# Kernel optimization log

Hardware: AMD Instinct MI355X
Metric: run time of the kernel (lower is better)

The kernel has to match this reference:

```python
import jax, jax.numpy as jnp
import numpy as np

B, L, H = 32, 512, 1024
H2 = H // 2          # split half = 512
D_ATTN = 64
EPS = 1e-5


def setup_inputs() -> dict:
    key = jax.random.key(0)
    ks = jax.random.split(key, 6)
    x = jax.random.normal(ks[0], (B, L, H), dtype=jnp.float32)
    # LayerNorm params (default torch init: weight=1, bias=0)
    ln_gamma = jnp.ones((H2,), jnp.float32)
    ln_beta = jnp.zeros((H2,), jnp.float32)
    # Toeplitz params (module inits w_vector=0, bias=1; use small random w for nontrivial math)
    w_vector = jax.random.normal(ks[1], (2 * L - 1,), jnp.float32) * 0.02
    t_bias = jnp.ones((L,), jnp.float32)
    # TinyAttention: kqv Linear(H2 -> 3*d_attn), proj Linear(d_attn -> H2)
    kqv_w = jax.random.normal(ks[2], (H2, 3 * D_ATTN), jnp.float32) * 0.02
    kqv_b = jnp.zeros((3 * D_ATTN,), jnp.float32)
    proj_w = jax.random.normal(ks[3], (D_ATTN, H2), jnp.float32) * 0.02
    proj_b = jnp.zeros((H2,), jnp.float32)
    return {"x": x, "ln_gamma": ln_gamma, "ln_beta": ln_beta,
            "w_vector": w_vector, "t_bias": t_bias,
            "kqv_w": kqv_w, "kqv_b": kqv_b, "proj_w": proj_w, "proj_b": proj_b}


def _toeplitz(w_vector):
    # Faithful replication of get_toeplitz(): pad, tile, trim, reshape, crop.
    r = w_vector.shape[0] // 2            # = L - 1
    t = jnp.pad(w_vector, (0, L))         # length 3L - 1
    t = jnp.tile(t, L)[:-L]               # length L * (3L - 2)
    t = t.reshape(L, 3 * L - 2)
    return t[:, r:-r]                      # [L, L]


def _tiny_attention(v, kqv_w, kqv_b, proj_w, proj_b):
    kqv = v @ kqv_w + kqv_b                        # [B, L, 3*d_attn]
    k, q, val = jnp.split(kqv, 3, axis=-1)         # chunk order: key, query, value
    scale = 1.0 / jnp.sqrt(jnp.float32(q.shape[-1]))
    scores = jnp.einsum('bqd,bkd->bqk', q, k) * scale
    soft = jax.nn.softmax(scores, axis=-1)
    head = jnp.einsum('bqk,bkd->bqd', soft, val)   # [B, L, d_attn]
    return head @ proj_w + proj_b                  # [B, L, H2]


def reference(x, ln_gamma, ln_beta, w_vector, t_bias, kqv_w, kqv_b, proj_w, proj_b):
    u, v = jnp.split(x, 2, axis=-1)                # each [B, L, H2]
    head = _tiny_attention(v, kqv_w, kqv_b, proj_w, proj_b)
    # LayerNorm over last dim
    mu = jnp.mean(v, axis=-1, keepdims=True)
    var = jnp.mean(jnp.square(v - mu), axis=-1, keepdims=True)
    vn = (v - mu) * jax.lax.rsqrt(var + EPS) * ln_gamma + ln_beta
    # spatial (Toeplitz) mixing: permute -> [B, H2, L], matmul [L, L], bias
    w_t = _toeplitz(w_vector)
    vm = jnp.einsum('blc,lm->bmc', vn, w_t.T).transpose(0, 2, 1)  # keep faithful: vp @ w_t
    vm = jnp.einsum('bcl,lm->bcm', vn.transpose(0, 2, 1), w_t) + t_bias
    v_out = vm.transpose(0, 2, 1) + head           # [B, L, H2]
    return u * v_out
```

## Files before the change

kernel.cpp:

```cpp
#include <hip/hip_runtime.h>
#include <math.h>

#define NB 32
#define LL 512
#define HH 1024
#define H2 512
#define DA 64

typedef unsigned int u32;
typedef unsigned short u16;
typedef __bf16 bf16x8 __attribute__((ext_vector_type(8)));
typedef float f32x4 __attribute__((ext_vector_type(4)));
typedef u16 u16x8 __attribute__((ext_vector_type(8)));

__device__ __forceinline__ u16 f2bu(float f) {
    u32 u = __builtin_bit_cast(u32, f);
    u = (u + 0x7fff + ((u >> 16) & 1)) >> 16;
    return (u16)u;
}

__device__ __forceinline__ float b2f(u16 u) {
    u32 v = (u32)u << 16;
    return __builtin_bit_cast(float, v);
}

__device__ __forceinline__ void async_cp16(const void* g, void* l) {
    __builtin_amdgcn_global_load_lds(
        (const __attribute__((address_space(1))) u32*)g,
        (__attribute__((address_space(3))) u32*)l, 16, 0, 0);
}

__global__ void prep_kernel(const float* __restrict__ wv,
                            const float* __restrict__ kqvw,
                            const float* __restrict__ projw,
                            u16* __restrict__ wt, u16* __restrict__ kqvwT,
                            u16* __restrict__ projwT) {
    int e = blockIdx.x * 256 + threadIdx.x;
    if (e < 262144) {
        int m = e >> 9, l = e & 511;
        wt[e] = f2bu(wv[511 + m - l]);
    } else if (e < 262144 + 98304) {
        int i = e - 262144;
        int n = i >> 9, k = i & 511;
        kqvwT[i] = f2bu(kqvw[(size_t)k * 192 + n]);
    } else {
        int i = e - 360448;
        int c = i >> 6, d = i & 63;
        projwT[i] = f2bu(projw[(size_t)d * 512 + c]);
    }
}

__global__ __launch_bounds__(256, 2)
void v_kernel(const float* __restrict__ x,
              const u16* __restrict__ kqvwT, const float* __restrict__ kqvb,
              const float* __restrict__ gamma, const float* __restrict__ beta,
              u16* __restrict__ vnT,
              u16* __restrict__ qb, u16* __restrict__ kb, u16* __restrict__ vT) {
    __shared__ u16 Af[32 * 64 * 8];
    __shared__ u16 Bs_[2][192 * 32];
    __shared__ float MU[32], RS[32];
    int blk = blockIdx.x, t = threadIdx.x;
    int R0 = blk * 32, b = R0 >> 9, l0 = R0 & 511;
    int lane = t & 63, wid = t >> 6;
    int l15 = lane & 15, q16 = lane >> 4, q8 = q16 * 8;
    int wm = (wid & 1) * 16, wn = (wid >> 1) * 96;
    const float* xg = x + (size_t)R0 * HH + H2;

    int arow = t >> 3, af4 = t & 7;
    int sgl = af4 >> 1;
    int shalf = (af4 & 1) * 4;

    float s1 = 0.f, s2 = 0.f;
    float4 av;
    f32x4 acc[6] = {};

#pragma unroll
    for (int s = 0; s < 3; ++s) {
        int ci = t + s * 256;
        int grow = ci >> 2, gcol = ((ci & 3) ^ (grow & 3)) << 3;
        async_cp16(kqvwT + (size_t)grow * 512 + gcol, &Bs_[0][ci * 8]);
    }
    av = *(const float4*)(xg + (size_t)arow * HH + af4 * 4);
    {
        s1 += av.x + av.y + av.z + av.w;
        s2 += av.x * av.x + av.y * av.y + av.z * av.z + av.w * av.w;
        ushort4 pk;
        pk.x = f2bu(av.x); pk.y = f2bu(av.y);
        pk.z = f2bu(av.z); pk.w = f2bu(av.w);
        int slot = sgl ^ (arow & 7);
        *(ushort4*)(&Af[(arow * 64 + slot) * 8 + shalf]) = pk;
    }
    __syncthreads();

    for (int it = 0; it < 16; ++it) {
        int nx = it + 1, nb = nx & 1, cb = it & 1;
        if (it < 15) {
            int k0n = nx * 32;
            av = *(const float4*)(xg + (size_t)arow * HH + k0n + af4 * 4);
#pragma unroll
            for (int s = 0; s < 3; ++s) {
                int ci = t + s * 256;
                int grow = ci >> 2, gcol = ((ci & 3) ^ (grow & 3)) << 3;
                async_cp16(kqvwT + (size_t)grow * 512 + k0n + gcol, &Bs_[nb][ci * 8]);
            }
        }
        const u16* Bp = &Bs_[cb][0];
        {
            int row = wm + l15;
            int g = (it * 4 + q16) ^ (row & 7);
            bf16x8 a = *(const bf16x8*)(&Af[(row * 64 + g) * 8]);
#pragma unroll
            for (int j = 0; j < 6; ++j) {
                int n = wn + j * 16 + l15;
                bf16x8 bb = *(const bf16x8*)(Bp + (n * 4 + (q16 ^ (n & 3))) * 8);
                acc[j] = __builtin_amdgcn_mfma_f32_16x16x32_bf16(a, bb, acc[j], 0, 0, 0);
            }
        }
        if (it < 15) {
            s1 += av.x + av.y + av.z + av.w;
            s2 += av.x * av.x + av.y * av.y + av.z * av.z + av.w * av.w;
            ushort4 pk;
            pk.x = f2bu(av.x); pk.y = f2bu(av.y);
            pk.z = f2bu(av.z); pk.w = f2bu(av.w);
            int slot = (nx * 4 + sgl) ^ (arow & 7);
            *(ushort4*)(&Af[(arow * 64 + slot) * 8 + shalf]) = pk;
        }
        __syncthreads();
    }

    s1 += __shfl_xor(s1, 1); s2 += __shfl_xor(s2, 1);
    s1 += __shfl_xor(s1, 2); s2 += __shfl_xor(s2, 2);
    s1 += __shfl_xor(s1, 4); s2 += __shfl_xor(s2, 4);
    if ((t & 7) == 0) {
        float mu = s1 * (1.0f / H2);
        float rstd = rsqrtf(s2 * (1.0f / H2) - mu * mu + 1e-5f);
        MU[arow] = mu; RS[arow] = rstd;
    }

    u16* Ks = &Bs_[0][0];
    u16* Qs = &Bs_[0][2048];
    u16* Vs = &Bs_[1][0];
    int rq = q16 * 4;
#pragma unroll
    for (int j = 0; j < 6; ++j) {
        int n = wn + j * 16 + l15;
        float bias = kqvb[n];
#pragma unroll
        for (int rr = 0; rr < 4; ++rr) {
            int m = wm + rq + rr;
            u16 hv = f2bu(acc[j][rr] + bias);
            if (n < 64)       Ks[m * 64 + n] = hv;
            else if (n < 128) Qs[m * 64 + (n - 64)] = hv;
            else              Vs[(n - 128) * 40 + m] = hv;
        }
    }
    __syncthreads();
    {
        size_t base = (size_t)R0 * 64 + t * 8;
        *(uint4*)(kb + base) = *(const uint4*)(Ks + t * 8);
        *(uint4*)(qb + base) = *(const uint4*)(Qs + t * 8);
        int d = t >> 2, ls = (t & 3) * 8;
        u16* vd = vT + ((size_t)(b * 64 + d)) * 512 + l0 + ls;
        *(uint4*)(vd) = *(const uint4*)(Vs + d * 40 + ls);
    }

#pragma unroll
    for (int cc = 0; cc < 2; ++cc) {
        int c = t + cc * 256;
        float ga = gamma[c], be = beta[c];
        u16* d0 = vnT + ((size_t)(b * H2 + c)) * LL + l0;
        int gbase = c >> 3, coff = c & 7;
#pragma unroll
        for (int lc = 0; lc < 4; ++lc) {
            u16x8 o0;
#pragma unroll
            for (int li = 0; li < 8; ++li) {
                int l = lc * 8 + li;
                u16 w = Af[(l * 64 + (gbase ^ (l & 7))) * 8 + coff];
                o0[li] = f2bu((b2f(w) - MU[l]) * RS[l] * ga + be);
            }
            *(u16x8*)(d0 + lc * 8) = o0;
        }
    }
}

#define VLD 136
__global__ __launch_bounds__(256, 4)
void attn_kernel(const u16* __restrict__ qb, const u16* __restrict__ kb,
                 const u16* __restrict__ vT, u16* __restrict__ head) {
    __shared__ u16 Ps[4 * 16 * VLD];
    __shared__ float Osh[4][16 * 65];
    __shared__ float Msh[4][16], Lsh[4][16];
    int b = blockIdx.y, q0 = blockIdx.x * 16;
    int t = threadIdx.x, lane = t & 63, w = t >> 6;
    int l15 = lane & 15, q16 = lane >> 4, q8 = q16 * 8;
    int kc = w * 128;
    const u16* qg = qb + (size_t)b * LL * DA;
    const u16* kg = kb + (size_t)b * LL * DA;
    const u16* vg = vT + (size_t)b * DA * LL;

    bf16x8 aq[2];
#pragma unroll
    for (int s = 0; s < 2; ++s)
        aq[s] = *(const bf16x8*)(qg + (size_t)(q0 + l15) * DA + s * 32 + q8);

    f32x4 sc[8] = {};
#pragma unroll
    for (int j = 0; j < 8; ++j) {
#pragma unroll
        for (int s = 0; s < 2; ++s) {
            bf16x8 bk = *(const bf16x8*)(kg + (size_t)(kc + j * 16 + l15) * DA + s * 32 + q8);
            sc[j] = __builtin_amdgcn_mfma_f32_16x16x32_bf16(aq[s], bk, sc[j], 0, 0, 0);
        }
    }
    float mx[4], sm[4];
#pragma unroll
    for (int j = 0; j < 8; ++j)
#pragma unroll
        for (int rr = 0; rr < 4; ++rr) sc[j][rr] *= 0.125f;
#pragma unroll
    for (int rr = 0; rr < 4; ++rr) {
        float m0 = sc[0][rr];
#pragma unroll
        for (int j = 1; j < 8; ++j) m0 = fmaxf(m0, sc[j][rr]);
        m0 = fmaxf(m0, __shfl_xor(m0, 1));
        m0 = fmaxf(m0, __shfl_xor(m0, 2));
        m0 = fmaxf(m0, __shfl_xor(m0, 4));
        m0 = fmaxf(m0, __shfl_xor(m0, 8));
        mx[rr] = m0;
    }
#pragma unroll
    for (int j = 0; j < 8; ++j)
#pragma unroll
        for (int rr = 0; rr < 4; ++rr) sc[j][rr] = __expf(sc[j][rr] - mx[rr]);
#pragma unroll
    for (int rr = 0; rr < 4; ++rr) {
        float s0 = sc[0][rr];
#pragma unroll
        for (int j = 1; j < 8; ++j) s0 += sc[j][rr];
        s0 += __shfl_xor(s0, 1);
        s0 += __shfl_xor(s0, 2);
        s0 += __shfl_xor(s0, 4);
        s0 += __shfl_xor(s0, 8);
        sm[rr] = s0;
    }
    u16* Pw = Ps + w * 16 * VLD;
#pragma unroll
    for (int j = 0; j < 8; ++j)
#pragma unroll
        for (int rr = 0; rr < 4; ++rr)
            Pw[(q16 * 4 + rr) * VLD + j * 16 + l15] = f2bu(sc[j][rr]);
    f32x4 o[4] = {};
#pragma unroll
    for (int kt = 0; kt < 4; ++kt) {
        bf16x8 ap = *(const bf16x8*)(Pw + l15 * VLD + kt * 32 + q8);
#pragma unroll
        for (int j = 0; j < 4; ++j) {
            bf16x8 bv = *(const bf16x8*)(vg + (size_t)(j * 16 + l15) * LL + kc + kt * 32 + q8);
            o[j] = __builtin_amdgcn_mfma_f32_16x16x32_bf16(ap, bv, o[j], 0, 0, 0);
        }
    }
#pragma unroll
    for (int j = 0; j < 4; ++j)
#pragma unroll
        for (int rr = 0; rr < 4; ++rr)
            Osh[w][(q16 * 4 + rr) * 65 + j * 16 + l15] = o[j][rr];
    if (l15 == 0) {
#pragma unroll
        for (int rr = 0; rr < 4; ++rr) {
            Msh[w][q16 * 4 + rr] = mx[rr];
            Lsh[w][q16 * 4 + rr] = sm[rr];
        }
    }
    __syncthreads();
    int qq = t >> 4, dg = (t & 15) * 4;
    float m0 = Msh[0][qq], m1 = Msh[1][qq], m2 = Msh[2][qq], m3 = Msh[3][qq];
    float ms = fmaxf(fmaxf(m0, m1), fmaxf(m2, m3));
    float f0 = __expf(m0 - ms), f1 = __expf(m1 - ms), f2 = __expf(m2 - ms), f3 = __expf(m3 - ms);
    float lst = Lsh[0][qq] * f0 + Lsh[1][qq] * f1 + Lsh[2][qq] * f2 + Lsh[3][qq] * f3;
    float inv = 1.0f / lst;
    ushort4 res;
    u16* rp = (u16*)&res;
#pragma unroll
    for (int i = 0; i < 4; ++i) {
        int idx = qq * 65 + dg + i;
        float a = Osh[0][idx] * f0 + Osh[1][idx] * f1 + Osh[2][idx] * f2 + Osh[3][idx] * f3;
        rp[i] = f2bu(a * inv);
    }
    *(ushort4*)(head + (size_t)(b * LL + q0 + qq) * DA + dg) = res;
}

__device__ __forceinline__ void mfma_tile64(const u16* As, const u16* Bs,
                                            f32x4 acc[4][4], int wm, int wn,
                                            int l15, int q16) {
    int s7 = l15 & 7;
#pragma unroll
    for (int kk = 0; kk < 2; ++kk) {
        int j0 = kk * 4 + q16;
        bf16x8 a[4], bv[4];
#pragma unroll
        for (int i = 0; i < 4; ++i) {
            int row = wm + i * 16 + l15;
            a[i] = *(const bf16x8*)(As + (row * 8 + (j0 ^ s7)) * 8);
        }
#pragma unroll
        for (int j = 0; j < 4; ++j) {
            int row = wn + j * 16 + l15;
            bv[j] = *(const bf16x8*)(Bs + (row * 8 + (j0 ^ s7)) * 8);
        }
#pragma unroll
        for (int i = 0; i < 4; ++i)
#pragma unroll
            for (int j = 0; j < 4; ++j)
                acc[i][j] = __builtin_amdgcn_mfma_f32_16x16x32_bf16(a[i], bv[j], acc[i][j], 0, 0, 0);
    }
}

__device__ __forceinline__ void stage_pair(const u16* A, const u16* B, int ldk,
                                           int koff, u16* Ad, u16* Bd, int t) {
#pragma unroll
    for (int s = 0; s < 4; ++s) {
        int ci = t + s * 256;
        int grow = ci >> 3, gcol = ((ci & 7) ^ (grow & 7)) << 3;
        async_cp16(A + (size_t)grow * ldk + koff + gcol, Ad + ci * 8);
        async_cp16(B + (size_t)grow * ldk + koff + gcol, Bd + ci * 8);
    }
}

__global__ __launch_bounds__(256, 2)
void mix_kernel(const u16* __restrict__ wt,
                const u16* __restrict__ vnT,
                const u16* __restrict__ headb,
                const u16* __restrict__ projwT,
                const float* __restrict__ x,
                const float* __restrict__ tbias,
                const float* __restrict__ projb,
                float* __restrict__ out) {
    __shared__ u16 SMEM[4][128 * 64];
    u16* As0 = SMEM[0]; u16* As1 = SMEM[1];
    u16* Bs0 = SMEM[2]; u16* Bs1 = SMEM[3];
    int lid = blockIdx.x;
    int p8 = lid & 7, rest = lid >> 3;
    int mi = rest & 3, pair = (rest >> 2) * 8 + p8;
    int b = pair >> 2, m0 = mi * 128, c0 = (pair & 3) * 128;
    int t = threadIdx.x, lane = t & 63, wid = t >> 6;
    int wm = (wid >> 1) * 64, wn = (wid & 1) * 64;
    int l15 = lane & 15, q16 = lane >> 4;
    f32x4 acc[4][4] = {};
    const u16* Ag = wt + (size_t)m0 * 512;
    const u16* Bg = vnT + ((size_t)b * H2 + c0) * 512;
    const u16* Hg = headb + ((size_t)b * LL + m0) * DA;
    const u16* Pg = projwT + (size_t)c0 * DA;

    stage_pair(Ag, Bg, 512, 0, As0, Bs0, t);
    __syncthreads();

    for (int it = 0; it < 9; ++it) {
        int nx = it + 1;
        if (nx < 8)
            stage_pair(Ag, Bg, 512, nx * 64, (nx & 1) ? As1 : As0,
                       (nx & 1) ? Bs1 : Bs0, t);
        else if (nx == 8)
            stage_pair(Hg, Pg, 64, 0, As0, Bs0, t);
        mfma_tile64((it & 1) ? As1 : As0, (it & 1) ? Bs1 : Bs0,
                    acc, wm, wn, l15, q16);
        __syncthreads();
    }

    float* Acc = (float*)&SMEM[0][0];
    int rq = q16 * 4;
#pragma unroll
    for (int i = 0; i < 4; ++i)
#pragma unroll
        for (int j = 0; j < 4; ++j)
#pragma unroll
            for (int rr = 0; rr < 4; ++rr)
                Acc[(wm + i * 16 + rq + rr) * 128 + (wn + j * 16 + l15)] = acc[i][j][rr];
    __syncthreads();
    {
        int cq = (t & 31) * 4, rg = (t >> 5) * 16;
        float4 pj = *(const float4*)(projb + c0 + cq);
#pragma unroll
        for (int rr3 = 0; rr3 < 16; ++rr3) {
            int mrow = rg + rr3;
            int m = m0 + mrow;
            float tb = tbias[m];
            float4 a4 = *(const float4*)(Acc + mrow * 128 + cq);
            float4 xv = *(const float4*)(x + ((size_t)b * LL + m) * HH + c0 + cq);
            float4 o;
            o.x = xv.x * (a4.x + tb + pj.x);
            o.y = xv.y * (a4.y + tb + pj.y);
            o.z = xv.z * (a4.z + tb + pj.z);
            o.w = xv.w * (a4.w + tb + pj.w);
            *(float4*)(out + ((size_t)b * LL + m) * H2 + c0 + cq) = o;
        }
    }
}

extern "C" void kernel_launch(void* const* d_in, const int* in_sizes, int n_in,
                              void* d_out, int out_size, void* d_ws, size_t ws_size,
                              hipStream_t stream) {
    (void)in_sizes; (void)n_in; (void)out_size; (void)ws_size;
    const float* x     = (const float*)d_in[0];
    const float* gamma = (const float*)d_in[1];
    const float* beta  = (const float*)d_in[2];
    const float* wv    = (const float*)d_in[3];
    const float* tb    = (const float*)d_in[4];
    const float* kqvw  = (const float*)d_in[5];
    const float* kqvb  = (const float*)d_in[6];
    const float* projw = (const float*)d_in[7];
    const float* projb = (const float*)d_in[8];
    float* out = (float*)d_out;

    u16* vnT_bf  = (u16*)d_ws;
    u16* qb      = vnT_bf + (size_t)NB * LL * H2;
    u16* kb      = qb + (size_t)NB * LL * DA;
    u16* vTb     = kb + (size_t)NB * LL * DA;
    u16* head_bf = vTb + (size_t)NB * LL * DA;
    u16* wt_bf   = head_bf + (size_t)NB * LL * DA;
    u16* kqvwT   = wt_bf + 512 * 512;
    u16* projwT  = kqvwT + 192 * 512;

    prep_kernel <<<1536, 256, 0, stream>>>(wv, kqvw, projw, wt_bf, kqvwT, projwT);
    v_kernel    <<<512, 256, 0, stream>>>(x, kqvwT, kqvb, gamma, beta,
                                          vnT_bf, qb, kb, vTb);
    attn_kernel <<<dim3(32, NB), 256, 0, stream>>>(qb, kb, vTb, head_bf);
    mix_kernel  <<<512, 256, 0, stream>>>(wt_bf, vnT_bf, head_bf, projwT,
                                          x, tb, projb, out);
}
```

Measured before the change: 171.4 us.

## Restructure v_kernel: 512 threads, upfront x row load, 64-wide K steps

v_kernel now launches 512 threads per block instead of 256. Each thread loads its whole 32-float slice of x up front, computes the LayerNorm sums and writes bf16 into shared memory before the GEMM. The GEMM loop then runs 8 iterations of K=64 instead of 16 of K=32, with 8 waves each computing 48 output columns. This cuts the number of barriers, adds memory-level parallelism for the x loads, and spreads the epilogue writes across more threads. In exchange, the B double buffer in shared memory doubles in size and register pressure rises under the (512,4) launch bound.

```diff
diff --git a/kernel.cpp b/kernel.cpp
--- a/kernel.cpp
+++ b/kernel.cpp
@@ -50,80 +50,75 @@
     }
 }
 
-__global__ __launch_bounds__(256, 2)
+__global__ __launch_bounds__(512, 4)
 void v_kernel(const float* __restrict__ x,
               const u16* __restrict__ kqvwT, const float* __restrict__ kqvb,
               const float* __restrict__ gamma, const float* __restrict__ beta,
               u16* __restrict__ vnT,
               u16* __restrict__ qb, u16* __restrict__ kb, u16* __restrict__ vT) {
     __shared__ u16 Af[32 * 64 * 8];
-    __shared__ u16 Bs_[2][192 * 32];
-    __shared__ float MU[32], RS[32];
+    __shared__ u16 Bs_[2][192 * 64];
     int blk = blockIdx.x, t = threadIdx.x;
     int R0 = blk * 32, b = R0 >> 9, l0 = R0 & 511;
     int lane = t & 63, wid = t >> 6;
-    int l15 = lane & 15, q16 = lane >> 4, q8 = q16 * 8;
-    int wm = (wid & 1) * 16, wn = (wid >> 1) * 96;
+    int l15 = lane & 15, q16 = lane >> 4;
+    int wm = (wid & 1) * 16, wn = (wid >> 1) * 48;
     const float* xg = x + (size_t)R0 * HH + H2;
 
-    int arow = t >> 3, af4 = t & 7;
-    int sgl = af4 >> 1;
-    int shalf = (af4 & 1) * 4;
+#pragma unroll
+    for (int s = 0; s < 3; ++s) {
+        int ci = t + s * 512;
+        int grow = ci >> 3, gcol = ((ci & 7) ^ (grow & 7)) << 3;
+        async_cp16(kqvwT + (size_t)grow * 512 + gcol, &Bs_[0][ci * 8]);
+    }
+    int row = t >> 4, seg = t & 15;
+    const float* xr = xg + (size_t)row * HH + seg * 32;
+    float4 xv[8];
+#pragma unroll
+    for (int i = 0; i < 8; ++i) xv[i] = *(const float4*)(xr + i * 4);
 
     float s1 = 0.f, s2 = 0.f;
-    float4 av;
-    f32x4 acc[6] = {};
-
-#pragma unroll
-    for (int s = 0; s < 3; ++s) {
-        int ci = t + s * 256;
-        int grow = ci >> 2, gcol = ((ci & 3) ^ (grow & 3)) << 3;
-        async_cp16(kqvwT + (size_t)grow * 512 + gcol, &Bs_[0][ci * 8]);
-    }
-    av = *(const float4*)(xg + (size_t)arow * HH + af4 * 4);
-    {
-        s1 += av.x + av.y + av.z + av.w;
-        s2 += av.x * av.x + av.y * av.y + av.z * av.z + av.w * av.w;
+    int r7 = row & 7;
+#pragma unroll
+    for (int i = 0; i < 8; ++i) {
+        float4 v = xv[i];
+        s1 += v.x + v.y + v.z + v.w;
+        s2 += v.x * v.x + v.y * v.y + v.z * v.z + v.w * v.w;
+        int g = seg * 4 + (i >> 1);
+        int slot = g ^ r7;
         ushort4 pk;
-        pk.x = f2bu(av.x); pk.y = f2bu(av.y);
-        pk.z = f2bu(av.z); pk.w = f2bu(av.w);
-        int slot = sgl ^ (arow & 7);
-        *(ushort4*)(&Af[(arow * 64 + slot) * 8 + shalf]) = pk;
+        pk.x = f2bu(v.x); pk.y = f2bu(v.y);
+        pk.z = f2bu(v.z); pk.w = f2bu(v.w);
+        *(ushort4*)(&Af[(row * 64 + slot) * 8 + (i & 1) * 4]) = pk;
     }
     __syncthreads();
 
-    for (int it = 0; it < 16; ++it) {
-        int nx = it + 1, nb = nx & 1, cb = it & 1;
-        if (it < 15) {
-            int k0n = nx * 32;
-            av = *(const float4*)(xg + (size_t)arow * HH + k0n + af4 * 4);
+    f32x4 acc[3] = {};
+    int rowA = wm + l15, rA7 = rowA & 7;
+    for (int it = 0; it < 8; ++it) {
+        int cb = it & 1;
+        if (it < 7) {
+            int k0n = (it + 1) * 64;
 #pragma unroll
             for (int s = 0; s < 3; ++s) {
-                int ci = t + s * 256;
-                int grow = ci >> 2, gcol = ((ci & 3) ^ (grow & 3)) << 3;
-                async_cp16(kqvwT + (size_t)grow * 512 + k0n + gcol, &Bs_[nb][ci * 8]);
+                int ci = t + s * 512;
+                int grow = ci >> 3, gcol = ((ci & 7) ^ (grow & 7)) << 3;
+                async_cp16(kqvwT + (size_t)grow * 512 + k0n + gcol,
+                           &Bs_[cb ^ 1][ci * 8]);
             }
         }
         const u16* Bp = &Bs_[cb][0];
-        {
-            int row = wm + l15;
-            int g = (it * 4 + q16) ^ (row & 7);
-            bf16x8 a = *(const bf16x8*)(&Af[(row * 64 + g) * 8]);
-#pragma unroll
-            for (int j = 0; j < 6; ++j) {
+#pragma unroll
+        for (int kk = 0; kk < 2; ++kk) {
+            int j0 = kk * 4 + q16;
+            int g = (it * 8 + j0) ^ rA7;
+            bf16x8 a = *(const bf16x8*)(&Af[(rowA * 64 + g) * 8]);
+#pragma unroll
+            for (int j = 0; j < 3; ++j) {
                 int n = wn + j * 16 + l15;
-                bf16x8 bb = *(const bf16x8*)(Bp + (n * 4 + (q16 ^ (n & 3))) * 8);
+                bf16x8 bb = *(const bf16x8*)(Bp + (n * 8 + (j0 ^ (n & 7))) * 8);
                 acc[j] = __builtin_amdgcn_mfma_f32_16x16x32_bf16(a, bb, acc[j], 0, 0, 0);
             }
-        }
-        if (it < 15) {
-            s1 += av.x + av.y + av.z + av.w;
-            s2 += av.x * av.x + av.y * av.y + av.z * av.z + av.w * av.w;
-            ushort4 pk;
-            pk.x = f2bu(av.x); pk.y = f2bu(av.y);
-            pk.z = f2bu(av.z); pk.w = f2bu(av.w);
-            int slot = (nx * 4 + sgl) ^ (arow & 7);
-            *(ushort4*)(&Af[(arow * 64 + slot) * 8 + shalf]) = pk;
         }
         __syncthreads();
     }
@@ -131,10 +126,13 @@
     s1 += __shfl_xor(s1, 1); s2 += __shfl_xor(s2, 1);
     s1 += __shfl_xor(s1, 2); s2 += __shfl_xor(s2, 2);
     s1 += __shfl_xor(s1, 4); s2 += __shfl_xor(s2, 4);
-    if ((t & 7) == 0) {
+    s1 += __shfl_xor(s1, 8); s2 += __shfl_xor(s2, 8);
+    float* MU = (float*)(&Bs_[1][8192]);
+    float* RS = MU + 32;
+    if ((t & 15) == 0) {
         float mu = s1 * (1.0f / H2);
         float rstd = rsqrtf(s2 * (1.0f / H2) - mu * mu + 1e-5f);
-        MU[arow] = mu; RS[arow] = rstd;
+        MU[row] = mu; RS[row] = rstd;
     }
 
     u16* Ks = &Bs_[0][0];
@@ -142,7 +140,7 @@
     u16* Vs = &Bs_[1][0];
     int rq = q16 * 4;
 #pragma unroll
-    for (int j = 0; j < 6; ++j) {
+    for (int j = 0; j < 3; ++j) {
         int n = wn + j * 16 + l15;
         float bias = kqvb[n];
 #pragma unroll
@@ -155,18 +153,20 @@
         }
     }
     __syncthreads();
+    if (t < 256) {
+        *(uint4*)(kb + (size_t)R0 * 64 + t * 8) = *(const uint4*)(Ks + t * 8);
+    } else {
+        int u = t - 256;
+        *(uint4*)(qb + (size_t)R0 * 64 + u * 8) = *(const uint4*)(Qs + u * 8);
+    }
     {
-        size_t base = (size_t)R0 * 64 + t * 8;
-        *(uint4*)(kb + base) = *(const uint4*)(Ks + t * 8);
-        *(uint4*)(qb + base) = *(const uint4*)(Qs + t * 8);
-        int d = t >> 2, ls = (t & 3) * 8;
-        u16* vd = vT + ((size_t)(b * 64 + d)) * 512 + l0 + ls;
-        *(uint4*)(vd) = *(const uint4*)(Vs + d * 40 + ls);
-    }
-
-#pragma unroll
-    for (int cc = 0; cc < 2; ++cc) {
-        int c = t + cc * 256;
+        int d = t >> 3, ls = (t & 7) * 4;
+        *(ushort4*)(vT + ((size_t)(b * 64 + d)) * 512 + l0 + ls) =
+            *(const ushort4*)(Vs + d * 40 + ls);
+    }
+
+    {
+        int c = t;
         float ga = gamma[c], be = beta[c];
         u16* d0 = vnT + ((size_t)(b * H2 + c)) * LL + l0;
         int gbase = c >> 3, coff = c & 7;
@@ -422,7 +422,7 @@
     u16* projwT  = kqvwT + 192 * 512;
 
     prep_kernel <<<1536, 256, 0, stream>>>(wv, kqvw, projw, wt_bf, kqvwT, projwT);
-    v_kernel    <<<512, 256, 0, stream>>>(x, kqvwT, kqvb, gamma, beta,
+    v_kernel    <<<512, 512, 0, stream>>>(x, kqvwT, kqvb, gamma, beta,
                                           vnT_bf, qb, kb, vTb);
     attn_kernel <<<dim3(32, NB), 256, 0, stream>>>(qb, kb, vTb, head_bf);
     mix_kernel  <<<512, 256, 0, stream>>>(wt_bf, vnT_bf, head_bf, projwT,
```

Result: no change. 169.4 us (-1.2%).
